# Optimization experiments

Measured on AMD Instinct MI355X. Metric: run time of the kernel, lower is better.

Reference implementation:

```python
import jax, jax.numpy as jnp
import numpy as np

B, L, D = 8, 1024, 1024
H = 16
HD = D // H  # 64
R = 8


def setup_inputs() -> dict:
    key = jax.random.key(0)
    ks = jax.random.split(key, 12)
    s = 1.0 / np.sqrt(D)
    return {
        "x": jax.random.normal(ks[0], (B, L, D), dtype=jnp.float32),
        "Wq": jax.random.normal(ks[1], (D, D), dtype=jnp.float32) * s,
        "bq": jnp.zeros((D,), dtype=jnp.float32),
        "Wk": jax.random.normal(ks[2], (D, D), dtype=jnp.float32) * s,
        "bk": jnp.zeros((D,), dtype=jnp.float32),
        "Wv": jax.random.normal(ks[3], (D, D), dtype=jnp.float32) * s,
        "bv": jnp.zeros((D,), dtype=jnp.float32),
        "Wo": jax.random.normal(ks[4], (D, D), dtype=jnp.float32) * s,
        "bo": jnp.zeros((D,), dtype=jnp.float32),
        "Wrel": jax.random.normal(ks[5], (H, R), dtype=jnp.float32) * (1.0 / np.sqrt(H)),
        "brel": jnp.zeros((R,), dtype=jnp.float32),
    }


def reference(x, Wq, bq, Wk, bk, Wv, bv, Wo, bo, Wrel, brel):
    # Standard MHA with need_weights=True: full [B,H,L,L] attention matrix.
    def heads(t):  # [B,L,D] -> [B,H,L,HD]
        return t.reshape(B, L, H, HD).transpose(0, 2, 1, 3)

    q = heads(x @ Wq + bq)
    k = heads(x @ Wk + bk)
    v = heads(x @ Wv + bv)

    scores = jnp.einsum('bhld,bhmd->bhlm', q, k) / jnp.sqrt(jnp.float32(HD))
    attn = jax.nn.softmax(scores, axis=-1)  # [B,H,L,L]

    ctx = jnp.einsum('bhlm,bhmd->bhld', attn, v)
    ctx = ctx.transpose(0, 2, 1, 3).reshape(B, L, D)
    output = ctx @ Wo + bo  # [B,L,D]

    # head_patterns: mean of attention weights over (L, L) -> [B, H]
    head_patterns = attn.mean(axis=(2, 3))
    relation_scores = head_patterns @ Wrel + brel  # [B,R]
    return output, relation_scores
```

## Files before the change

### kernel.cpp

```cpp
#include <hip/hip_runtime.h>
#include <math.h>

using f32x4  = __attribute__((ext_vector_type(4))) float;
using bf16x8 = __attribute__((ext_vector_type(8))) short;
using us8    = __attribute__((ext_vector_type(8))) unsigned short;
using us4    = __attribute__((ext_vector_type(4))) unsigned short;

static __device__ __forceinline__ unsigned short f32_bf16(float f) {
    unsigned int u = __float_as_uint(f);
    u += 0x7fffu + ((u >> 16) & 1u);
    return (unsigned short)(u >> 16);
}

static __device__ __forceinline__ float fast_exp2(float x) {
    return __builtin_amdgcn_exp2f(x);
}

static __device__ __forceinline__ unsigned int bf16pk(float lo, float hi) {
    unsigned int r;
    asm("v_cvt_pk_bf16_f32 %0, %1, %2" : "=v"(r) : "v"(lo), "v"(hi));
    return r;
}

#define GLOADLDS16(src, dst)                                                          \
    __builtin_amdgcn_global_load_lds(                                                 \
        (const __attribute__((address_space(1))) void*)(src),                         \
        (__attribute__((address_space(3))) void*)(dst), 16, 0, 0)

__global__ __launch_bounds__(256) void conv_x_kernel(const float* __restrict__ x,
                                                     unsigned short* __restrict__ xb) {
    const int i = blockIdx.x * 256 + threadIdx.x;
    const float4 v = ((const float4*)x)[i];
    us4 o;
    o.x = f32_bf16(v.x); o.y = f32_bf16(v.y); o.z = f32_bf16(v.z); o.w = f32_bf16(v.w);
    ((us4*)xb)[i] = o;
}

__global__ __launch_bounds__(256) void conv_wT_kernel(
    const float* __restrict__ Wq, const float* __restrict__ Wk,
    const float* __restrict__ Wv, const float* __restrict__ Wo,
    unsigned short* __restrict__ wqkvT, unsigned short* __restrict__ woT) {
    __shared__ float t[32][33];
    const int z = blockIdx.z;
    const float* W = (z == 0) ? Wq : (z == 1) ? Wk : (z == 2) ? Wv : Wo;
    unsigned short* dst = (z < 3) ? (wqkvT + (size_t)z * 1024 * 1024) : woT;
    const int bx = blockIdx.x * 32, by = blockIdx.y * 32;
    const int tx = threadIdx.x & 31, ty = threadIdx.x >> 5;
#pragma unroll
    for (int i = ty; i < 32; i += 8)
        t[i][tx] = W[(size_t)(by + i) * 1024 + bx + tx];
    __syncthreads();
#pragma unroll
    for (int i = ty; i < 32; i += 8)
        dst[(size_t)(bx + i) * 1024 + by + tx] = f32_bf16(t[tx][i]);
}

template<int MODE>
__global__ __launch_bounds__(256) void gemm_bt_kernel(
    const unsigned short* __restrict__ A, const unsigned short* __restrict__ Bt,
    const float* __restrict__ bias_q, const float* __restrict__ bias_k,
    const float* __restrict__ bias_v,
    unsigned short* __restrict__ qkv, float* __restrict__ cout) {
    constexpr int K = 1024;
    __shared__ unsigned short As[128 * 64];
    __shared__ unsigned short Bs[128 * 64];
    const int tid = threadIdx.x;
    const int wid = tid >> 6, lane = tid & 63;
    const int bm = blockIdx.x * 128, bn = blockIdx.y * 128;
    const int wr = wid >> 1, wc = wid & 1;
    const int l15 = lane & 15, lg = lane >> 4;
    const int srow = lane >> 3;
    const int schunk = (lane & 7) ^ srow;

    f32x4 acc[4][4] = {};

    for (int kt = 0; kt < K / 64; ++kt) {
#pragma unroll
        for (int i = 0; i < 4; ++i) {
            const int li = wid * 4 + i;
            const unsigned short* sa =
                A + (size_t)(bm + li * 8 + srow) * K + kt * 64 + schunk * 8;
            GLOADLDS16(sa, &As[li * 512]);
            const unsigned short* sb =
                Bt + (size_t)(bn + li * 8 + srow) * K + kt * 64 + schunk * 8;
            GLOADLDS16(sb, &Bs[li * 512]);
        }
        __syncthreads();
#pragma unroll
        for (int ks = 0; ks < 2; ++ks) {
            bf16x8 af[4], bfr[4];
#pragma unroll
            for (int m = 0; m < 4; ++m) {
                const int row = wr * 64 + m * 16 + l15;
                const int c = (ks * 4 + lg) ^ (row & 7);
                af[m] = *(const bf16x8*)&As[row * 64 + c * 8];
            }
#pragma unroll
            for (int n = 0; n < 4; ++n) {
                const int row = wc * 64 + n * 16 + l15;
                const int c = (ks * 4 + lg) ^ (row & 7);
                bfr[n] = *(const bf16x8*)&Bs[row * 64 + c * 8];
            }
#pragma unroll
            for (int m = 0; m < 4; ++m)
#pragma unroll
                for (int n = 0; n < 4; ++n)
                    acc[m][n] = __builtin_amdgcn_mfma_f32_16x16x32_bf16(
                        bfr[n], af[m], acc[m][n], 0, 0, 0);
        }
        __syncthreads();
    }
    if constexpr (MODE == 0) {
        const int which = bn >> 10;
        const int hnb = (bn & 1023) + wc * 64;
        const float* bias = (which == 0) ? bias_q : (which == 1) ? bias_k : bias_v;
        if (which == 2) {
#pragma unroll
            for (int m = 0; m < 4; ++m) {
                const int gm = bm + wr * 64 + m * 16 + l15;
                const int b_ = gm >> 10, li2 = gm & 1023;
#pragma unroll
                for (int n = 0; n < 4; ++n) {
                    const int hn0 = hnb + n * 16 + lg * 4;
                    const float4 bb = *(const float4*)&bias[hn0];
                    const float vv[4] = {acc[m][n][0] + bb.x, acc[m][n][1] + bb.y,
                                         acc[m][n][2] + bb.z, acc[m][n][3] + bb.w};
#pragma unroll
                    for (int r = 0; r < 4; ++r) {
                        const int hn = hn0 + r;
                        qkv[16777216 +
                            ((size_t)(b_ * 16 + (hn >> 6)) * 64 + (hn & 63)) * 1024 +
                            li2] = f32_bf16(vv[r]);
                    }
                }
            }
        } else {
            const float qs = (which == 0) ? 0.125f * 1.44269504088896f : 1.0f;
#pragma unroll
            for (int m = 0; m < 4; ++m) {
                const int gm = bm + wr * 64 + m * 16 + l15;
                const size_t rowbase =
                    (((size_t)which * 128 + (gm >> 10) * 16) * 1024 + (gm & 1023)) * 64;
#pragma unroll
                for (int n = 0; n < 4; ++n) {
                    const int hn0 = hnb + n * 16 + lg * 4;
                    const float4 bb = *(const float4*)&bias[hn0];
                    const unsigned int w01 = bf16pk((acc[m][n][0] + bb.x) * qs,
                                                    (acc[m][n][1] + bb.y) * qs);
                    const unsigned int w23 = bf16pk((acc[m][n][2] + bb.z) * qs,
                                                    (acc[m][n][3] + bb.w) * qs);
                    uint2 t; t.x = w01; t.y = w23;
                    *(uint2*)&qkv[rowbase + (size_t)(hn0 >> 6) * 65536 + (hn0 & 63)] = t;
                }
            }
        }
    } else {
#pragma unroll
        for (int m = 0; m < 4; ++m) {
            const int gm = bm + wr * 64 + m * 16 + l15;
#pragma unroll
            for (int n = 0; n < 4; ++n) {
                const int gn0 = bn + wc * 64 + n * 16 + lg * 4;
                const float4 bb = *(const float4*)&bias_q[gn0];
                float4 o;
                o.x = acc[m][n][0] + bb.x; o.y = acc[m][n][1] + bb.y;
                o.z = acc[m][n][2] + bb.z; o.w = acc[m][n][3] + bb.w;
                *(float4*)&cout[(size_t)gm * 1024 + gn0] = o;
            }
        }
    }
}

__global__ __launch_bounds__(512) void attn_kernel(
    const unsigned short* __restrict__ qkv, unsigned short* __restrict__ ctx) {
    __shared__ unsigned short Ks[2][4096];
    __shared__ unsigned short VTs[2][4096];
    __shared__ unsigned short Ps[8][1024];
    const int bh = blockIdx.x, qt = blockIdx.y;
    const int b = bh >> 4, h = bh & 15;
    const unsigned short* Qp  = qkv + (size_t)bh * 65536;
    const unsigned short* Kp  = qkv + 8388608  + (size_t)bh * 65536;
    const unsigned short* VTp = qkv + 16777216 + (size_t)bh * 65536;
    const int tid = threadIdx.x, wid = tid >> 6, lane = tid & 63;
    const int l15 = lane & 15, lg = lane >> 4;
    const int q0 = qt * 128 + wid * 16;
    const int srow = lane >> 3;
    const int schunk = (lane & 7) ^ srow;

    bf16x8 qf[2];
#pragma unroll
    for (int ks = 0; ks < 2; ++ks)
        qf[ks] = *(const bf16x8*)(Qp + (size_t)(q0 + l15) * 64 + ks * 32 + lg * 8);

    f32x4 oacc[4] = {};
    float lrow = 0.f;

    int koff[4][2], poff_r[2], poff_w[4];
#pragma unroll
    for (int nf = 0; nf < 4; ++nf)
#pragma unroll
        for (int ks = 0; ks < 2; ++ks) {
            const int row = nf * 16 + l15;
            koff[nf][ks] = row * 64 + (((ks * 4 + lg) ^ (row & 7)) * 8);
        }
#pragma unroll
    for (int ks = 0; ks < 2; ++ks)
        poff_r[ks] = l15 * 64 + (((ks * 4 + lg) ^ (l15 & 7)) * 8);
#pragma unroll
    for (int nf = 0; nf < 4; ++nf) {
        const int cchunk = nf * 2 + (lg >> 1);
        poff_w[nf] = l15 * 64 + ((cchunk ^ (l15 & 7)) * 8) + (lg & 1) * 4;
    }
    unsigned short* Pw = &Ps[wid][0];

#define ATTN_STAGE(KT, BB)                                                            \
    do {                                                                              \
        GLOADLDS16(Kp + (size_t)((KT) * 64 + wid * 8 + srow) * 64 + schunk * 8,       \
                   &Ks[BB][wid * 512]);                                               \
        GLOADLDS16(VTp + (size_t)(wid * 8 + srow) * 1024 + (KT) * 64 + schunk * 8,    \
                   &VTs[BB][wid * 512]);                                              \
    } while (0)

    ATTN_STAGE(0, 0);
    for (int kt = 0; kt < 16; ++kt) {
        const int cur = kt & 1;
        if (kt < 15) {
            ATTN_STAGE(kt + 1, cur ^ 1);
            asm volatile("s_waitcnt vmcnt(2)" ::: "memory");
        } else {
            asm volatile("s_waitcnt vmcnt(0)" ::: "memory");
        }
        __builtin_amdgcn_s_barrier();

        const unsigned short* Kb = &Ks[cur][0];
        const unsigned short* Vb = &VTs[cur][0];

        f32x4 sacc[4] = {};
        __builtin_amdgcn_s_setprio(1);
#pragma unroll
        for (int ks = 0; ks < 2; ++ks)
#pragma unroll
            for (int nf = 0; nf < 4; ++nf) {
                const bf16x8 kf = *(const bf16x8*)&Kb[koff[nf][ks]];
                sacc[nf] = __builtin_amdgcn_mfma_f32_16x16x32_bf16(
                    kf, qf[ks], sacc[nf], 0, 0, 0);
            }
        __builtin_amdgcn_s_setprio(0);

        float rsa = 0.f, rsb = 0.f;
#pragma unroll
        for (int nf = 0; nf < 4; ++nf) {
            const float p0 = fast_exp2(sacc[nf][0]);
            const float p1 = fast_exp2(sacc[nf][1]);
            const float p2 = fast_exp2(sacc[nf][2]);
            const float p3 = fast_exp2(sacc[nf][3]);
            rsa += p0 + p1; rsb += p2 + p3;
            uint2 t; t.x = bf16pk(p0, p1); t.y = bf16pk(p2, p3);
            *(uint2*)&Pw[poff_w[nf]] = t;
        }
        lrow += rsa + rsb;

        __builtin_amdgcn_s_setprio(1);
#pragma unroll
        for (int ks = 0; ks < 2; ++ks) {
            const bf16x8 pf = *(const bf16x8*)&Pw[poff_r[ks]];
#pragma unroll
            for (int nf = 0; nf < 4; ++nf) {
                const bf16x8 vf = *(const bf16x8*)&Vb[koff[nf][ks]];
                oacc[nf] = __builtin_amdgcn_mfma_f32_16x16x32_bf16(
                    vf, pf, oacc[nf], 0, 0, 0);
            }
        }
        __builtin_amdgcn_s_setprio(0);

        __builtin_amdgcn_s_barrier();
    }
#undef ATTN_STAGE

    lrow += __shfl_xor(lrow, 16);
    lrow += __shfl_xor(lrow, 32);
    const float rl = 1.0f / lrow;

#pragma unroll
    for (int nf = 0; nf < 4; ++nf) {
        uint2 t;
        t.x = bf16pk(oacc[nf][0] * rl, oacc[nf][1] * rl);
        t.y = bf16pk(oacc[nf][2] * rl, oacc[nf][3] * rl);
        *(uint2*)&ctx[((size_t)(b * 1024 + q0 + l15)) * 1024 + h * 64 + nf * 16 +
                      lg * 4] = t;
    }
}

__global__ __launch_bounds__(64) void relation_kernel(
    const float* __restrict__ Wrel, const float* __restrict__ brel,
    float* __restrict__ out) {
    const int t = threadIdx.x;
    const int r = t & 7;
    float s = 0.f;
#pragma unroll
    for (int hh = 0; hh < 16; ++hh) s += Wrel[hh * 8 + r];
    out[8 * 1024 * 1024 + t] = s * (1.0f / 1024.0f) + brel[r];
}

extern "C" void kernel_launch(void* const* d_in, const int* in_sizes, int n_in,
                              void* d_out, int out_size, void* d_ws, size_t ws_size,
                              hipStream_t stream) {
    (void)in_sizes; (void)n_in; (void)out_size; (void)ws_size;
    const float* x    = (const float*)d_in[0];
    const float* Wq   = (const float*)d_in[1];
    const float* bq   = (const float*)d_in[2];
    const float* Wk   = (const float*)d_in[3];
    const float* bk   = (const float*)d_in[4];
    const float* Wv   = (const float*)d_in[5];
    const float* bv   = (const float*)d_in[6];
    const float* Wo   = (const float*)d_in[7];
    const float* bo   = (const float*)d_in[8];
    const float* Wrel = (const float*)d_in[9];
    const float* brel = (const float*)d_in[10];
    float* out = (float*)d_out;

    char* ws = (char*)d_ws;
    unsigned short* xb    = (unsigned short*)ws;
    unsigned short* wqkvT = (unsigned short*)(ws + 16777216);
    unsigned short* woT   = (unsigned short*)(ws + 16777216 + 6291456);
    unsigned short* qkv   = (unsigned short*)(ws + 16777216 + 6291456 + 2097152);
    unsigned short* ctx   = xb;

    conv_x_kernel<<<8192, 256, 0, stream>>>(x, xb);
    conv_wT_kernel<<<dim3(32, 32, 4), 256, 0, stream>>>(Wq, Wk, Wv, Wo, wqkvT, woT);
    gemm_bt_kernel<0><<<dim3(64, 24), 256, 0, stream>>>(
        xb, wqkvT, bq, bk, bv, qkv, nullptr);
    attn_kernel<<<dim3(128, 8), 512, 0, stream>>>(qkv, ctx);
    gemm_bt_kernel<1><<<dim3(64, 8), 256, 0, stream>>>(
        ctx, woT, bo, nullptr, nullptr, nullptr, out);
    relation_kernel<<<1, 64, 0, stream>>>(Wrel, brel, out);
}
```

Before: 164.0 us.

## Double-buffer GEMM LDS tiles with 128x256 blocks and interleaved prefetch

The bf16 GEMM used for the QKV and output projections now runs 512 threads on 128x256 output tiles, with double-buffered LDS for A and B. The next k-tile's global-to-LDS loads are issued between MFMA groups, and s_setprio is raised around the MFMAs. The goal is to hide global load latency behind compute and to reuse each A tile across twice as many columns. In exchange the block uses 96KB of LDS and the grid has half as many blocks. That cuts occupancy and the number of blocks per CU, and adds extra barriers inside each k-tile.

Measured after the change: 174.1 us. 1.06x slower.

```diff
diff --git a/kernel.cpp b/kernel.cpp
--- a/kernel.cpp
+++ b/kernel.cpp
@@ -56,60 +56,104 @@
 }
 
 template<int MODE>
-__global__ __launch_bounds__(256) void gemm_bt_kernel(
+__global__ __launch_bounds__(512) void gemm_bt_kernel(
     const unsigned short* __restrict__ A, const unsigned short* __restrict__ Bt,
     const float* __restrict__ bias_q, const float* __restrict__ bias_k,
     const float* __restrict__ bias_v,
     unsigned short* __restrict__ qkv, float* __restrict__ cout) {
     constexpr int K = 1024;
-    __shared__ unsigned short As[128 * 64];
-    __shared__ unsigned short Bs[128 * 64];
+    __shared__ unsigned short As[2][128 * 64];
+    __shared__ unsigned short Bs[2][256 * 64];
     const int tid = threadIdx.x;
     const int wid = tid >> 6, lane = tid & 63;
-    const int bm = blockIdx.x * 128, bn = blockIdx.y * 128;
-    const int wr = wid >> 1, wc = wid & 1;
+    const int bm = blockIdx.x * 128, bn = blockIdx.y * 256;
+    const int wr = wid >> 2, wc = wid & 3;
     const int l15 = lane & 15, lg = lane >> 4;
-    const int srow = lane >> 3;
-    const int schunk = (lane & 7) ^ srow;
+    const int srow = tid >> 3;
+    const int schunk = (tid & 7) ^ (srow & 7);
 
     f32x4 acc[4][4] = {};
 
-    for (int kt = 0; kt < K / 64; ++kt) {
-#pragma unroll
-        for (int i = 0; i < 4; ++i) {
-            const int li = wid * 4 + i;
-            const unsigned short* sa =
-                A + (size_t)(bm + li * 8 + srow) * K + kt * 64 + schunk * 8;
-            GLOADLDS16(sa, &As[li * 512]);
-            const unsigned short* sb =
-                Bt + (size_t)(bn + li * 8 + srow) * K + kt * 64 + schunk * 8;
-            GLOADLDS16(sb, &Bs[li * 512]);
-        }
-        __syncthreads();
-#pragma unroll
-        for (int ks = 0; ks < 2; ++ks) {
-            bf16x8 af[4], bfr[4];
-#pragma unroll
-            for (int m = 0; m < 4; ++m) {
-                const int row = wr * 64 + m * 16 + l15;
-                const int c = (ks * 4 + lg) ^ (row & 7);
-                af[m] = *(const bf16x8*)&As[row * 64 + c * 8];
-            }
-#pragma unroll
-            for (int n = 0; n < 4; ++n) {
-                const int row = wc * 64 + n * 16 + l15;
-                const int c = (ks * 4 + lg) ^ (row & 7);
-                bfr[n] = *(const bf16x8*)&Bs[row * 64 + c * 8];
-            }
-#pragma unroll
-            for (int m = 0; m < 4; ++m)
-#pragma unroll
-                for (int n = 0; n < 4; ++n)
-                    acc[m][n] = __builtin_amdgcn_mfma_f32_16x16x32_bf16(
-                        bfr[n], af[m], acc[m][n], 0, 0, 0);
-        }
-        __syncthreads();
-    }
+    const unsigned short* aptr = A + (size_t)(bm + srow) * K + schunk * 8;
+    const unsigned short* bptr = Bt + (size_t)(bn + srow) * K + schunk * 8;
+
+#define STAGE_A(T, BUF, LI)                                                           \
+    GLOADLDS16(aptr + (size_t)(LI) * 64 * K + (T) * 64, &As[BUF][(LI)*4096 + wid*512])
+#define STAGE_B(T, BUF, LI)                                                           \
+    GLOADLDS16(bptr + (size_t)(LI) * 64 * K + (T) * 64, &Bs[BUF][(LI)*4096 + wid*512])
+
+    const int abase = (wr * 64 + l15) * 64;
+    const int bbase = (wc * 64 + l15) * 64;
+    const int cb0 = ((lg) ^ (l15 & 7)) * 8;
+    const int cb1 = ((4 + lg) ^ (l15 & 7)) * 8;
+
+    STAGE_A(0, 0, 0); STAGE_A(0, 0, 1);
+    STAGE_B(0, 0, 0); STAGE_B(0, 0, 1); STAGE_B(0, 0, 2); STAGE_B(0, 0, 3);
+    asm volatile("s_waitcnt vmcnt(0)" ::: "memory");
+    __builtin_amdgcn_s_barrier();
+
+    for (int t = 0; t < 16; ++t) {
+        const int cur = t & 1, nxt = cur ^ 1;
+        const unsigned short* Ab = &As[cur][0];
+        const unsigned short* Bb = &Bs[cur][0];
+        const bool pf = (t < 15);
+        bf16x8 af0, af1, bfr[4];
+
+#pragma unroll
+        for (int n = 0; n < 4; ++n) bfr[n] = *(const bf16x8*)&Bb[bbase + n * 1024 + cb0];
+        af0 = *(const bf16x8*)&Ab[abase + cb0];
+        af1 = *(const bf16x8*)&Ab[abase + 1024 + cb0];
+        if (pf) { STAGE_A(t + 1, nxt, 0); STAGE_A(t + 1, nxt, 1); }
+        __builtin_amdgcn_s_setprio(1);
+#pragma unroll
+        for (int n = 0; n < 4; ++n) {
+            acc[0][n] = __builtin_amdgcn_mfma_f32_16x16x32_bf16(bfr[n], af0, acc[0][n], 0, 0, 0);
+            acc[1][n] = __builtin_amdgcn_mfma_f32_16x16x32_bf16(bfr[n], af1, acc[1][n], 0, 0, 0);
+        }
+        __builtin_amdgcn_s_setprio(0);
+        __builtin_amdgcn_s_barrier();
+
+        af0 = *(const bf16x8*)&Ab[abase + 2048 + cb0];
+        af1 = *(const bf16x8*)&Ab[abase + 3072 + cb0];
+        if (pf) { STAGE_B(t + 1, nxt, 0); STAGE_B(t + 1, nxt, 1); }
+        __builtin_amdgcn_s_setprio(1);
+#pragma unroll
+        for (int n = 0; n < 4; ++n) {
+            acc[2][n] = __builtin_amdgcn_mfma_f32_16x16x32_bf16(bfr[n], af0, acc[2][n], 0, 0, 0);
+            acc[3][n] = __builtin_amdgcn_mfma_f32_16x16x32_bf16(bfr[n], af1, acc[3][n], 0, 0, 0);
+        }
+        __builtin_amdgcn_s_setprio(0);
+        __builtin_amdgcn_s_barrier();
+
+#pragma unroll
+        for (int n = 0; n < 4; ++n) bfr[n] = *(const bf16x8*)&Bb[bbase + n * 1024 + cb1];
+        af0 = *(const bf16x8*)&Ab[abase + cb1];
+        af1 = *(const bf16x8*)&Ab[abase + 1024 + cb1];
+        if (pf) { STAGE_B(t + 1, nxt, 2); STAGE_B(t + 1, nxt, 3); }
+        __builtin_amdgcn_s_setprio(1);
+#pragma unroll
+        for (int n = 0; n < 4; ++n) {
+            acc[0][n] = __builtin_amdgcn_mfma_f32_16x16x32_bf16(bfr[n], af0, acc[0][n], 0, 0, 0);
+            acc[1][n] = __builtin_amdgcn_mfma_f32_16x16x32_bf16(bfr[n], af1, acc[1][n], 0, 0, 0);
+        }
+        __builtin_amdgcn_s_setprio(0);
+        __builtin_amdgcn_s_barrier();
+
+        af0 = *(const bf16x8*)&Ab[abase + 2048 + cb1];
+        af1 = *(const bf16x8*)&Ab[abase + 3072 + cb1];
+        __builtin_amdgcn_s_setprio(1);
+#pragma unroll
+        for (int n = 0; n < 4; ++n) {
+            acc[2][n] = __builtin_amdgcn_mfma_f32_16x16x32_bf16(bfr[n], af0, acc[2][n], 0, 0, 0);
+            acc[3][n] = __builtin_amdgcn_mfma_f32_16x16x32_bf16(bfr[n], af1, acc[3][n], 0, 0, 0);
+        }
+        __builtin_amdgcn_s_setprio(0);
+        asm volatile("s_waitcnt vmcnt(0)" ::: "memory");
+        __builtin_amdgcn_s_barrier();
+    }
+#undef STAGE_A
+#undef STAGE_B
+
     if constexpr (MODE == 0) {
         const int which = bn >> 10;
         const int hnb = (bn & 1023) + wc * 64;
@@ -149,8 +193,8 @@
                                                     (acc[m][n][1] + bb.y) * qs);
                     const unsigned int w23 = bf16pk((acc[m][n][2] + bb.z) * qs,
                                                     (acc[m][n][3] + bb.w) * qs);
-                    uint2 t; t.x = w01; t.y = w23;
-                    *(uint2*)&qkv[rowbase + (size_t)(hn0 >> 6) * 65536 + (hn0 & 63)] = t;
+                    uint2 t2; t2.x = w01; t2.y = w23;
+                    *(uint2*)&qkv[rowbase + (size_t)(hn0 >> 6) * 65536 + (hn0 & 63)] = t2;
                 }
             }
         }
@@ -328,10 +372,10 @@
 
     conv_x_kernel<<<8192, 256, 0, stream>>>(x, xb);
     conv_wT_kernel<<<dim3(32, 32, 4), 256, 0, stream>>>(Wq, Wk, Wv, Wo, wqkvT, woT);
-    gemm_bt_kernel<0><<<dim3(64, 24), 256, 0, stream>>>(
+    gemm_bt_kernel<0><<<dim3(64, 12), 512, 0, stream>>>(
         xb, wqkvT, bq, bk, bv, qkv, nullptr);
     attn_kernel<<<dim3(128, 8), 512, 0, stream>>>(qkv, ctx);
-    gemm_bt_kernel<1><<<dim3(64, 8), 256, 0, stream>>>(
+    gemm_bt_kernel<1><<<dim3(64, 4), 512, 0, stream>>>(
         ctx, woT, bo, nullptr, nullptr, nullptr, out);
     relation_kernel<<<1, 64, 0, stream>>>(Wrel, brel, out);
 }
```

## Rewrite QKV GEMM with 256x256 tiles, double-buffered LDS and interleaved prefetch

Applied to the files above, without the earlier changes.

Replaces the templated QKV projection GEMM with a dedicated 512-thread kernel that uses 256x256 output tiles, double-buffered LDS, and prefetch of the next K-tile split into quarters that overlap with MFMA phases, with s_setprio around compute. Block indices are remapped so neighbouring blocks share B tiles for better L2 reuse. The goal is to hide global-to-LDS latency and raise arithmetic intensity in the dominant GEMM. The cost is 128KB of LDS per block and heavy register use, which limits occupancy, and the hand-tuned vmcnt waits are fragile.

New measurement: 169.4 us. 3.3% more time.

```diff
diff --git a/kernel.cpp b/kernel.cpp
--- a/kernel.cpp
+++ b/kernel.cpp
@@ -55,12 +55,189 @@
         dst[(size_t)(bx + i) * 1024 + by + tx] = f32_bf16(t[tx][i]);
 }
 
-template<int MODE>
-__global__ __launch_bounds__(256) void gemm_bt_kernel(
+__global__ __launch_bounds__(512, 2) void gemm_qkv_kernel(
     const unsigned short* __restrict__ A, const unsigned short* __restrict__ Bt,
     const float* __restrict__ bias_q, const float* __restrict__ bias_k,
-    const float* __restrict__ bias_v,
-    unsigned short* __restrict__ qkv, float* __restrict__ cout) {
+    const float* __restrict__ bias_v, unsigned short* __restrict__ qkv) {
+    constexpr int K = 1024;
+    __shared__ unsigned short As[2][256 * 64];
+    __shared__ unsigned short Bs[2][256 * 64];
+    const int tid = threadIdx.x;
+    const int wid = tid >> 6, lane = tid & 63;
+    const int l = blockIdx.x;
+    const int bm = (((l & 7) << 2) + ((l >> 3) & 3)) * 256;
+    const int by = l >> 5;
+    const int bn = by * 256;
+    const int wr = wid >> 2, wc = wid & 3;
+    const int l15 = lane & 15, lg = lane >> 4;
+    const int r8 = lane >> 3;
+    const int schunk = (lane & 7) ^ r8;
+
+    f32x4 acc[8][4] = {};
+
+    const unsigned short* aS = A  + (size_t)(bm + wid * 8 + r8) * K + schunk * 8;
+    const unsigned short* bS = Bt + (size_t)(bn + (wid >> 1) * 64 + (wid & 1) * 8 + r8) * K + schunk * 8;
+    const int adst = wid * 8 * 64;
+    const int bdst = ((wid >> 1) * 64 + (wid & 1) * 8) * 64;
+
+#define SA(a, T, BUF) GLOADLDS16(aS + (size_t)(a) * 64 * K + (T) * 64, \
+                                 &As[BUF][adst + (a) * 4096])
+#define SB(q, T, BUF) GLOADLDS16(bS + (size_t)(q) * 16 * K + (T) * 64, \
+                                 &Bs[BUF][bdst + (q) * 1024])
+
+    const int c0 = ((lg) ^ (l15 & 7)) * 8;
+    const int c1 = ((4 + lg) ^ (l15 & 7)) * 8;
+    const int arow = (wr * 128 + l15) * 64;
+    const int brow = (wc * 64 + l15) * 64;
+
+    SA(0, 0, 0); SA(2, 0, 0); SB(0, 0, 0); SB(1, 0, 0);
+    SB(2, 0, 0); SB(3, 0, 0); SA(1, 0, 0); SA(3, 0, 0);
+
+    for (int t = 0; t < 16; ++t) {
+        const int cur = t & 1, nxt = cur ^ 1;
+        const bool pf = (t < 15);
+        const unsigned short* Ab = &As[cur][0];
+        const unsigned short* Bb = &Bs[cur][0];
+        bf16x8 af[4][2], bfr[2][2];
+
+        asm volatile("s_waitcnt vmcnt(4)" ::: "memory");
+        __builtin_amdgcn_s_barrier();
+#pragma unroll
+        for (int mf = 0; mf < 4; ++mf) {
+            af[mf][0] = *(const bf16x8*)&Ab[arow + mf * 1024 + c0];
+            af[mf][1] = *(const bf16x8*)&Ab[arow + mf * 1024 + c1];
+        }
+#pragma unroll
+        for (int nf = 0; nf < 2; ++nf) {
+            bfr[nf][0] = *(const bf16x8*)&Bb[brow + nf * 1024 + c0];
+            bfr[nf][1] = *(const bf16x8*)&Bb[brow + nf * 1024 + c1];
+        }
+        if (pf) { SA(0, t + 1, nxt); SA(2, t + 1, nxt); }
+        __builtin_amdgcn_s_setprio(1);
+#pragma unroll
+        for (int ks = 0; ks < 2; ++ks)
+#pragma unroll
+            for (int mf = 0; mf < 4; ++mf)
+#pragma unroll
+                for (int nf = 0; nf < 2; ++nf)
+                    acc[mf][nf] = __builtin_amdgcn_mfma_f32_16x16x32_bf16(
+                        bfr[nf][ks], af[mf][ks], acc[mf][nf], 0, 0, 0);
+        __builtin_amdgcn_s_setprio(0);
+
+        if (pf) asm volatile("s_waitcnt vmcnt(4)" ::: "memory");
+        else    asm volatile("s_waitcnt vmcnt(2)" ::: "memory");
+        __builtin_amdgcn_s_barrier();
+#pragma unroll
+        for (int nf = 0; nf < 2; ++nf) {
+            bfr[nf][0] = *(const bf16x8*)&Bb[brow + (2 + nf) * 1024 + c0];
+            bfr[nf][1] = *(const bf16x8*)&Bb[brow + (2 + nf) * 1024 + c1];
+        }
+        if (pf) { SB(0, t + 1, nxt); SB(1, t + 1, nxt); }
+        __builtin_amdgcn_s_setprio(1);
+#pragma unroll
+        for (int ks = 0; ks < 2; ++ks)
+#pragma unroll
+            for (int mf = 0; mf < 4; ++mf)
+#pragma unroll
+                for (int nf = 0; nf < 2; ++nf)
+                    acc[mf][2 + nf] = __builtin_amdgcn_mfma_f32_16x16x32_bf16(
+                        bfr[nf][ks], af[mf][ks], acc[mf][2 + nf], 0, 0, 0);
+        __builtin_amdgcn_s_setprio(0);
+
+        if (pf) asm volatile("s_waitcnt vmcnt(4)" ::: "memory");
+        else    asm volatile("s_waitcnt vmcnt(0)" ::: "memory");
+        __builtin_amdgcn_s_barrier();
+#pragma unroll
+        for (int mf = 0; mf < 4; ++mf) {
+            af[mf][0] = *(const bf16x8*)&Ab[arow + 4096 + mf * 1024 + c0];
+            af[mf][1] = *(const bf16x8*)&Ab[arow + 4096 + mf * 1024 + c1];
+        }
+#pragma unroll
+        for (int nf = 0; nf < 2; ++nf) {
+            bfr[nf][0] = *(const bf16x8*)&Bb[brow + nf * 1024 + c0];
+            bfr[nf][1] = *(const bf16x8*)&Bb[brow + nf * 1024 + c1];
+        }
+        if (pf) { SB(2, t + 1, nxt); SB(3, t + 1, nxt); }
+        __builtin_amdgcn_s_setprio(1);
+#pragma unroll
+        for (int ks = 0; ks < 2; ++ks)
+#pragma unroll
+            for (int mf = 0; mf < 4; ++mf)
+#pragma unroll
+                for (int nf = 0; nf < 2; ++nf)
+                    acc[4 + mf][nf] = __builtin_amdgcn_mfma_f32_16x16x32_bf16(
+                        bfr[nf][ks], af[mf][ks], acc[4 + mf][nf], 0, 0, 0);
+        __builtin_amdgcn_s_setprio(0);
+
+        __builtin_amdgcn_s_barrier();
+#pragma unroll
+        for (int nf = 0; nf < 2; ++nf) {
+            bfr[nf][0] = *(const bf16x8*)&Bb[brow + (2 + nf) * 1024 + c0];
+            bfr[nf][1] = *(const bf16x8*)&Bb[brow + (2 + nf) * 1024 + c1];
+        }
+        if (pf) { SA(1, t + 1, nxt); SA(3, t + 1, nxt); }
+        __builtin_amdgcn_s_setprio(1);
+#pragma unroll
+        for (int ks = 0; ks < 2; ++ks)
+#pragma unroll
+            for (int mf = 0; mf < 4; ++mf)
+#pragma unroll
+                for (int nf = 0; nf < 2; ++nf)
+                    acc[4 + mf][2 + nf] = __builtin_amdgcn_mfma_f32_16x16x32_bf16(
+                        bfr[nf][ks], af[mf][ks], acc[4 + mf][2 + nf], 0, 0, 0);
+        __builtin_amdgcn_s_setprio(0);
+    }
+#undef SA
+#undef SB
+
+    const int which = bn >> 10;
+    const int hnb = (bn & 1023) + wc * 64;
+    const float* bias = (which == 0) ? bias_q : (which == 1) ? bias_k : bias_v;
+    if (which == 2) {
+#pragma unroll
+        for (int m = 0; m < 8; ++m) {
+            const int gm = bm + wr * 128 + m * 16 + l15;
+            const int b_ = gm >> 10, li2 = gm & 1023;
+#pragma unroll
+            for (int n = 0; n < 4; ++n) {
+                const int hn0 = hnb + n * 16 + lg * 4;
+                const float4 bb = *(const float4*)&bias[hn0];
+                const float vv[4] = {acc[m][n][0] + bb.x, acc[m][n][1] + bb.y,
+                                     acc[m][n][2] + bb.z, acc[m][n][3] + bb.w};
+#pragma unroll
+                for (int r = 0; r < 4; ++r) {
+                    const int hn = hn0 + r;
+                    qkv[16777216 +
+                        ((size_t)(b_ * 16 + (hn >> 6)) * 64 + (hn & 63)) * 1024 +
+                        li2] = f32_bf16(vv[r]);
+                }
+            }
+        }
+    } else {
+        const float qs = (which == 0) ? 0.125f * 1.44269504088896f : 1.0f;
+#pragma unroll
+        for (int m = 0; m < 8; ++m) {
+            const int gm = bm + wr * 128 + m * 16 + l15;
+            const size_t rowbase =
+                (((size_t)which * 128 + (gm >> 10) * 16) * 1024 + (gm & 1023)) * 64;
+#pragma unroll
+            for (int n = 0; n < 4; ++n) {
+                const int hn0 = hnb + n * 16 + lg * 4;
+                const float4 bb = *(const float4*)&bias[hn0];
+                const unsigned int w01 = bf16pk((acc[m][n][0] + bb.x) * qs,
+                                                (acc[m][n][1] + bb.y) * qs);
+                const unsigned int w23 = bf16pk((acc[m][n][2] + bb.z) * qs,
+                                                (acc[m][n][3] + bb.w) * qs);
+                uint2 t2; t2.x = w01; t2.y = w23;
+                *(uint2*)&qkv[rowbase + (size_t)(hn0 >> 6) * 65536 + (hn0 & 63)] = t2;
+            }
+        }
+    }
+}
+
+__global__ __launch_bounds__(256) void gemm_out_kernel(
+    const unsigned short* __restrict__ A, const unsigned short* __restrict__ Bt,
+    const float* __restrict__ bias, float* __restrict__ cout) {
     constexpr int K = 1024;
     __shared__ unsigned short As[128 * 64];
     __shared__ unsigned short Bs[128 * 64];
@@ -110,63 +287,17 @@
         }
         __syncthreads();
     }
-    if constexpr (MODE == 0) {
-        const int which = bn >> 10;
-        const int hnb = (bn & 1023) + wc * 64;
-        const float* bias = (which == 0) ? bias_q : (which == 1) ? bias_k : bias_v;
-        if (which == 2) {
-#pragma unroll
-            for (int m = 0; m < 4; ++m) {
-                const int gm = bm + wr * 64 + m * 16 + l15;
-                const int b_ = gm >> 10, li2 = gm & 1023;
-#pragma unroll
-                for (int n = 0; n < 4; ++n) {
-                    const int hn0 = hnb + n * 16 + lg * 4;
-                    const float4 bb = *(const float4*)&bias[hn0];
-                    const float vv[4] = {acc[m][n][0] + bb.x, acc[m][n][1] + bb.y,
-                                         acc[m][n][2] + bb.z, acc[m][n][3] + bb.w};
-#pragma unroll
-                    for (int r = 0; r < 4; ++r) {
-                        const int hn = hn0 + r;
-                        qkv[16777216 +
-                            ((size_t)(b_ * 16 + (hn >> 6)) * 64 + (hn & 63)) * 1024 +
-                            li2] = f32_bf16(vv[r]);
-                    }
-                }
-            }
-        } else {
-            const float qs = (which == 0) ? 0.125f * 1.44269504088896f : 1.0f;
-#pragma unroll
-            for (int m = 0; m < 4; ++m) {
-                const int gm = bm + wr * 64 + m * 16 + l15;
-                const size_t rowbase =
-                    (((size_t)which * 128 + (gm >> 10) * 16) * 1024 + (gm & 1023)) * 64;
-#pragma unroll
-                for (int n = 0; n < 4; ++n) {
-                    const int hn0 = hnb + n * 16 + lg * 4;
-                    const float4 bb = *(const float4*)&bias[hn0];
-                    const unsigned int w01 = bf16pk((acc[m][n][0] + bb.x) * qs,
-                                                    (acc[m][n][1] + bb.y) * qs);
-                    const unsigned int w23 = bf16pk((acc[m][n][2] + bb.z) * qs,
-                                                    (acc[m][n][3] + bb.w) * qs);
-                    uint2 t; t.x = w01; t.y = w23;
-                    *(uint2*)&qkv[rowbase + (size_t)(hn0 >> 6) * 65536 + (hn0 & 63)] = t;
-                }
-            }
-        }
-    } else {
-#pragma unroll
-        for (int m = 0; m < 4; ++m) {
-            const int gm = bm + wr * 64 + m * 16 + l15;
-#pragma unroll
-            for (int n = 0; n < 4; ++n) {
-                const int gn0 = bn + wc * 64 + n * 16 + lg * 4;
-                const float4 bb = *(const float4*)&bias_q[gn0];
-                float4 o;
-                o.x = acc[m][n][0] + bb.x; o.y = acc[m][n][1] + bb.y;
-                o.z = acc[m][n][2] + bb.z; o.w = acc[m][n][3] + bb.w;
-                *(float4*)&cout[(size_t)gm * 1024 + gn0] = o;
-            }
+#pragma unroll
+    for (int m = 0; m < 4; ++m) {
+        const int gm = bm + wr * 64 + m * 16 + l15;
+#pragma unroll
+        for (int n = 0; n < 4; ++n) {
+            const int gn0 = bn + wc * 64 + n * 16 + lg * 4;
+            const float4 bb = *(const float4*)&bias[gn0];
+            float4 o;
+            o.x = acc[m][n][0] + bb.x; o.y = acc[m][n][1] + bb.y;
+            o.z = acc[m][n][2] + bb.z; o.w = acc[m][n][3] + bb.w;
+            *(float4*)&cout[(size_t)gm * 1024 + gn0] = o;
         }
     }
 }
@@ -328,10 +459,8 @@
 
     conv_x_kernel<<<8192, 256, 0, stream>>>(x, xb);
     conv_wT_kernel<<<dim3(32, 32, 4), 256, 0, stream>>>(Wq, Wk, Wv, Wo, wqkvT, woT);
-    gemm_bt_kernel<0><<<dim3(64, 24), 256, 0, stream>>>(
-        xb, wqkvT, bq, bk, bv, qkv, nullptr);
+    gemm_qkv_kernel<<<384, 512, 0, stream>>>(xb, wqkvT, bq, bk, bv, qkv);
     attn_kernel<<<dim3(128, 8), 512, 0, stream>>>(qkv, ctx);
-    gemm_bt_kernel<1><<<dim3(64, 8), 256, 0, stream>>>(
-        ctx, woT, bo, nullptr, nullptr, nullptr, out);
+    gemm_out_kernel<<<dim3(64, 8), 256, 0, stream>>>(ctx, woT, bo, out);
     relation_kernel<<<1, 64, 0, stream>>>(Wrel, brel, out);
 }
```

## Double-buffer LDS tiles in projection GEMM to overlap global loads with MFMA

Applied to the files above, without the earlier changes.

The bf16 GEMM used for the QKV and output projections now keeps two LDS buffers for each of A and B. It prefetches the next K-tile with direct global-to-LDS loads while the current tile feeds the MFMAs, and needs only one barrier per iteration instead of two. It also reads all fragments for both k-substeps up front and raises wave priority around the MFMA block. The cost is twice the LDS use per block, which may lower occupancy, and more fragment registers.

New measurement: 170.2 us. 1.04x slower.

```diff
diff --git a/kernel.cpp b/kernel.cpp
--- a/kernel.cpp
+++ b/kernel.cpp
@@ -62,8 +62,8 @@
     const float* __restrict__ bias_v,
     unsigned short* __restrict__ qkv, float* __restrict__ cout) {
     constexpr int K = 1024;
-    __shared__ unsigned short As[128 * 64];
-    __shared__ unsigned short Bs[128 * 64];
+    __shared__ unsigned short As[2][128 * 64];
+    __shared__ unsigned short Bs[2][128 * 64];
     const int tid = threadIdx.x;
     const int wid = tid >> 6, lane = tid & 63;
     const int bm = blockIdx.x * 128, bn = blockIdx.y * 128;
@@ -74,42 +74,60 @@
 
     f32x4 acc[4][4] = {};
 
-    for (int kt = 0; kt < K / 64; ++kt) {
-#pragma unroll
-        for (int i = 0; i < 4; ++i) {
-            const int li = wid * 4 + i;
-            const unsigned short* sa =
-                A + (size_t)(bm + li * 8 + srow) * K + kt * 64 + schunk * 8;
-            GLOADLDS16(sa, &As[li * 512]);
-            const unsigned short* sb =
-                Bt + (size_t)(bn + li * 8 + srow) * K + kt * 64 + schunk * 8;
-            GLOADLDS16(sb, &Bs[li * 512]);
-        }
-        __syncthreads();
-#pragma unroll
-        for (int ks = 0; ks < 2; ++ks) {
-            bf16x8 af[4], bfr[4];
-#pragma unroll
-            for (int m = 0; m < 4; ++m) {
-                const int row = wr * 64 + m * 16 + l15;
+#define STAGE(T, BUF)                                                                 \
+    do {                                                                              \
+        _Pragma("unroll")                                                             \
+        for (int i = 0; i < 4; ++i) {                                                 \
+            const int li = wid * 4 + i;                    \
+            GLOADLDS16(A + (size_t)(bm + li * 8 + srow) * K + (T) * 64 + schunk * 8,  \
+                       &As[BUF][li * 512]);                                           \
+            GLOADLDS16(Bt + (size_t)(bn + li * 8 + srow) * K + (T) * 64 + schunk * 8, \
+                       &Bs[BUF][li * 512]);                                           \
+        }                                                                             \
+    } while (0)
+
+    STAGE(0, 0);
+    asm volatile("s_waitcnt vmcnt(0)" ::: "memory");
+    __builtin_amdgcn_s_barrier();
+
+    for (int kt = 0; kt < 16; ++kt) {
+        const int cur = kt & 1;
+        if (kt < 15) STAGE(kt + 1, cur ^ 1);
+
+        bf16x8 af[4][2], bfr[4][2];
+#pragma unroll
+        for (int m = 0; m < 4; ++m) {
+            const int row = wr * 64 + m * 16 + l15;
+#pragma unroll
+            for (int ks = 0; ks < 2; ++ks) {
                 const int c = (ks * 4 + lg) ^ (row & 7);
-                af[m] = *(const bf16x8*)&As[row * 64 + c * 8];
-            }
-#pragma unroll
-            for (int n = 0; n < 4; ++n) {
-                const int row = wc * 64 + n * 16 + l15;
+                af[m][ks] = *(const bf16x8*)&As[cur][row * 64 + c * 8];
+            }
+        }
+#pragma unroll
+        for (int n = 0; n < 4; ++n) {
+            const int row = wc * 64 + n * 16 + l15;
+#pragma unroll
+            for (int ks = 0; ks < 2; ++ks) {
                 const int c = (ks * 4 + lg) ^ (row & 7);
-                bfr[n] = *(const bf16x8*)&Bs[row * 64 + c * 8];
-            }
+                bfr[n][ks] = *(const bf16x8*)&Bs[cur][row * 64 + c * 8];
+            }
+        }
+        __builtin_amdgcn_s_setprio(1);
+#pragma unroll
+        for (int ks = 0; ks < 2; ++ks)
 #pragma unroll
             for (int m = 0; m < 4; ++m)
 #pragma unroll
                 for (int n = 0; n < 4; ++n)
                     acc[m][n] = __builtin_amdgcn_mfma_f32_16x16x32_bf16(
-                        bfr[n], af[m], acc[m][n], 0, 0, 0);
-        }
-        __syncthreads();
-    }
+                        bfr[n][ks], af[m][ks], acc[m][n], 0, 0, 0);
+        __builtin_amdgcn_s_setprio(0);
+        asm volatile("s_waitcnt vmcnt(0)" ::: "memory");
+        __builtin_amdgcn_s_barrier();
+    }
+#undef STAGE
+
     if constexpr (MODE == 0) {
         const int which = bn >> 10;
         const int hnb = (bn & 1023) + wc * 64;
@@ -149,8 +167,8 @@
                                                     (acc[m][n][1] + bb.y) * qs);
                     const unsigned int w23 = bf16pk((acc[m][n][2] + bb.z) * qs,
                                                     (acc[m][n][3] + bb.w) * qs);
-                    uint2 t; t.x = w01; t.y = w23;
-                    *(uint2*)&qkv[rowbase + (size_t)(hn0 >> 6) * 65536 + (hn0 & 63)] = t;
+                    uint2 t2; t2.x = w01; t2.y = w23;
+                    *(uint2*)&qkv[rowbase + (size_t)(hn0 >> 6) * 65536 + (hn0 & 63)] = t2;
                 }
             }
         }
```
